# Optimization experiments

Measured on AMD Instinct MI355X. Metric: run time of the kernel, lower is better.

The kernel has to match this reference:

```python
import jax, jax.numpy as jnp
import numpy as np

B = 16      # number of point clouds
N = 4096    # points per cloud (max after densify)
D = 3       # xyz


def setup_inputs() -> dict:
    key = jax.random.key(0)
    k1, k2 = jax.random.split(key)
    pred = jax.random.normal(k1, (B * N, D), dtype=jnp.float32)
    target = jax.random.normal(k2, (B * N, D), dtype=jnp.float32)
    # sorted segment ids, equal-sized clouds (faithful to to_dense_batch usage)
    batch = jnp.repeat(jnp.arange(B, dtype=jnp.int64), N)
    return {"pred": pred, "target": target, "batch": batch}


def to_dense_batch(x, batch, num_batches, max_n):
    # PyG to_dense_batch: scatter flat points into [B, max_n, D], zero-padded.
    ones = jnp.ones_like(batch)
    counts = jax.ops.segment_sum(ones, batch, num_segments=num_batches)
    offsets = jnp.concatenate([jnp.zeros((1,), batch.dtype), jnp.cumsum(counts)[:-1]])
    pos = jnp.arange(batch.shape[0], dtype=batch.dtype) - offsets[batch]
    dense = jnp.zeros((num_batches, max_n, x.shape[-1]), x.dtype)
    return dense.at[batch, pos].set(x)


def chamfer_distance(x, y):
    # squared-euclidean pairwise distances via the GEMM identity
    x2 = jnp.sum(x * x, axis=-1)                      # [B, N]
    y2 = jnp.sum(y * y, axis=-1)                      # [B, M]
    xy = jnp.einsum('bnd,bmd->bnm', x, y)             # [B, N, M]
    d = x2[:, :, None] + y2[:, None, :] - 2.0 * xy    # [B, N, M]
    cham_x = jnp.mean(jnp.min(d, axis=2), axis=1)     # mean over N of min over M
    cham_y = jnp.mean(jnp.min(d, axis=1), axis=1)     # mean over M of min over N
    # point_reduction='mean', batch_reduction='mean' (pytorch3d defaults)
    return jnp.mean(cham_x + cham_y)


def reference(pred, target, batch):
    x = to_dense_batch(pred, batch, B, N)
    y = to_dense_batch(target, batch, B, N)
    return chamfer_distance(x, y)
```

## Files before the change

### kernel.cpp

```cpp
#include <hip/hip_runtime.h>


namespace {

constexpr int kB = 16;
constexpr int kN = 4096;
constexpr int kPlane = kB * kN;
constexpr int kStage = 512;
constexpr int kNS = kN / kStage;
constexpr float kScale = 1.0f / (float)(kB * kN);

typedef short bf16x8 __attribute__((ext_vector_type(8)));
typedef float f32x4 __attribute__((ext_vector_type(4)));
typedef unsigned short u16;

__device__ inline u16 bf16_rn(float f) {
  union { float f; unsigned u; } v; v.f = f;
  unsigned r = v.u + 0x7fffu + ((v.u >> 16) & 1u);
  return (u16)(r >> 16);
}
__device__ inline float bf16_f(u16 h) {
  union { unsigned u; float f; } v; v.u = (unsigned)h << 16;
  return v.f;
}
__device__ inline unsigned pk2(u16 lo, u16 hi) {
  return (unsigned)lo | ((unsigned)hi << 16);
}

__global__ void init_out(float* out) { out[0] = 0.0f; }

__global__ __launch_bounds__(256) void cd_prep(
    const float* __restrict__ pred, const float* __restrict__ targ,
    u16* __restrict__ Apred, u16* __restrict__ Atarg,
    u16* __restrict__ Bpred, u16* __restrict__ Btarg,
    float* __restrict__ out) {
  const int p = blockIdx.x * 256 + threadIdx.x;
  if (p == 0) out[0] = 0.0f;
  const int cloud = p >> 12, q = p & (kN - 1);
  const int stg = q >> 9, pl = q & (kStage - 1);
  const size_t boff = (size_t)cloud * 65536 + (size_t)stg * 8192 + (size_t)pl * 8;
  const u16 one = 0x3F80;

  const float* srcs[2] = {pred, targ};
  u16* adsts[2] = {Apred, Atarg};
  u16* bdsts[2] = {Bpred, Btarg};
#pragma unroll
  for (int which = 0; which < 2; ++which) {
    const float a = srcs[which][3 * p], c = srcs[which][3 * p + 1],
                d = srcs[which][3 * p + 2];
    const u16 ah = bf16_rn(a), ch = bf16_rn(c), dh = bf16_rn(d);
    const u16 al = bf16_rn(a - bf16_f(ah));
    const u16 cl = bf16_rn(c - bf16_f(ch));
    const u16 dl = bf16_rn(d - bf16_f(dh));
    const float s2 = fmaf(a, a, fmaf(c, c, d * d));
    const u16 s2h = bf16_rn(s2);
    const u16 s2l = bf16_rn(s2 - bf16_f(s2h));
    {
      uint4 w0, w1;
      w0.x = pk2(ah, ch); w0.y = pk2(dh, al); w0.z = pk2(cl, dl); w0.w = pk2(ah, ch);
      w1.x = pk2(dh, al); w1.y = pk2(cl, dl); w1.z = pk2(s2h, s2l); w1.w = pk2(one, one);
      uint4* dst = reinterpret_cast<uint4*>(adsts[which] + (size_t)p * 16);
      dst[0] = w0; dst[1] = w1;
    }
    {
      const u16 nah = bf16_rn(-2.0f * bf16_f(ah));
      const u16 nch = bf16_rn(-2.0f * bf16_f(ch));
      const u16 ndh = bf16_rn(-2.0f * bf16_f(dh));
      const u16 nal = bf16_rn(-2.0f * bf16_f(al));
      const u16 ncl = bf16_rn(-2.0f * bf16_f(cl));
      const u16 ndl = bf16_rn(-2.0f * bf16_f(dl));
      uint4 w0, w1;
      w0.x = pk2(nah, nch); w0.y = pk2(ndh, nah); w0.z = pk2(nch, ndh); w0.w = pk2(nal, ncl);
      w1.x = pk2(ndl, nal); w1.y = pk2(ncl, ndl); w1.z = pk2(one, one); w1.w = pk2(s2h, s2l);
      *reinterpret_cast<uint4*>(bdsts[which] + boff) = w0;
      *reinterpret_cast<uint4*>(bdsts[which] + boff + 4096) = w1;
    }
  }
}

__global__ __launch_bounds__(256) void cd_mfma(
    const u16* __restrict__ Apred, const u16* __restrict__ Atarg,
    const u16* __restrict__ Bpred, const u16* __restrict__ Btarg,
    float* __restrict__ out) {
  __shared__ uint4 Blds4[2052];
  __shared__ float wsum[4];

  const int t = threadIdx.x;
  const int w = t >> 6, lane = t & 63;
  const int l15 = lane & 15, kg = lane >> 4;
  const bool act = (kg < 2);
  const int g = kg & 1;
  const int chunk = blockIdx.x;
  const int cloud = blockIdx.y;
  const int dir = blockIdx.z;
  const u16* __restrict__ A = dir ? Atarg : Apred;
  const u16* __restrict__ B = dir ? Bpred : Btarg;

  const int arow0 = cloud * kN + chunk * 128 + w * 32 + l15;
  union { uint4 u; bf16x8 v; } af0, af1;
  af0.u = make_uint4(0, 0, 0, 0);
  af1.u = make_uint4(0, 0, 0, 0);
  if (act) {
    af0.u = *reinterpret_cast<const uint4*>(A + (size_t)arow0 * 16 + g * 8);
    af1.u = *reinterpret_cast<const uint4*>(A + (size_t)(arow0 + 16) * 16 + g * 8);
  }

  const char* bcloud = (const char*)B + (size_t)cloud * 131072;
  char* ldsbase = (char*)Blds4;
#define STAGE(st, buf)                                                        \
  {                                                                           \
    const char* _src = bcloud + (size_t)(st) * 16384;                         \
    char* _dst = ldsbase + (buf) * 16384;                                     \
    _Pragma("unroll")                                                         \
    for (int i = 0; i < 4; ++i) {                                             \
      __builtin_amdgcn_global_load_lds(                                       \
          (const __attribute__((address_space(1))) void*)(_src +              \
              ((w * 4 + i) * 64 + lane) * 16),                                \
          (__attribute__((address_space(3))) void*)(_dst + (w * 4 + i) * 1024),\
          16, 0, 0);                                                          \
    }                                                                         \
  }

  const int rb0 = act ? (g * 8192 + l15 * 16) : 32768;
  const int rstep = act ? 256 : 0;
  const int bufstep = act ? 16384 : 0;

  f32x4 z4;
#pragma unroll
  for (int r = 0; r < 4; ++r) z4[r] = 0.0f;
  float rmin0[4], rmin1[4];
#pragma unroll
  for (int r = 0; r < 4; ++r) { rmin0[r] = 1e30f; rmin1[r] = 1e30f; }

  STAGE(0, 0);
  if (t == 0) Blds4[2048] = make_uint4(0, 0, 0, 0);
  __syncthreads();

  for (int st = 0; st < kNS; ++st) {
    if (st < kNS - 1) STAGE(st + 1, (st + 1) & 1);
    const char* pb = ldsbase + rb0 + (st & 1) * bufstep;
#pragma unroll 4
    for (int jt = 0; jt < kStage / 16; ++jt) {
      union { uint4 u; bf16x8 v; } bu;
      bu.u = *reinterpret_cast<const uint4*>(pb);
      pb += rstep;
      const f32x4 s0 =
          __builtin_amdgcn_mfma_f32_16x16x32_bf16(af0.v, bu.v, z4, 0, 0, 0);
      const f32x4 s1 =
          __builtin_amdgcn_mfma_f32_16x16x32_bf16(af1.v, bu.v, z4, 0, 0, 0);
#pragma unroll
      for (int r = 0; r < 4; ++r) {
        rmin0[r] = fminf(rmin0[r], s0[r]);
        rmin1[r] = fminf(rmin1[r], s1[r]);
      }
    }
    __syncthreads();
  }
#undef STAGE

#pragma unroll
  for (int sh = 1; sh < 16; sh <<= 1) {
#pragma unroll
    for (int r = 0; r < 4; ++r) {
      rmin0[r] = fminf(rmin0[r], __shfl_xor(rmin0[r], sh, 64));
      rmin1[r] = fminf(rmin1[r], __shfl_xor(rmin1[r], sh, 64));
    }
  }
  float s = 0.0f;
#pragma unroll
  for (int r = 0; r < 4; ++r) s += rmin0[r] + rmin1[r];
  s = (l15 == 0) ? s : 0.0f;
  s += __shfl_xor(s, 16, 64);
  s += __shfl_xor(s, 32, 64);
  if (lane == 0) wsum[w] = s;
  __syncthreads();
  if (t == 0)
    atomicAdd(out, (wsum[0] + wsum[1] + wsum[2] + wsum[3]) * kScale);
}

template <int KX>
__global__ __launch_bounds__(256) void chamfer_direct(
    const float* __restrict__ pred, const float* __restrict__ targ,
    float* __restrict__ out) {
  __shared__ float4 tA[128], tB[128];
  const int t = threadIdx.x;
  const int xb = blockIdx.x, b = blockIdx.y, dir = blockIdx.z;
  const float* __restrict__ X = dir ? targ : pred;
  const float* __restrict__ Y = dir ? pred : targ;
  float2 xx2[KX], xy2[KX], xz2[KX];
  float x2[KX], mn[KX];
  const int ibase = b * kN + xb * (256 * KX) + t;
#pragma unroll
  for (int k = 0; k < KX; ++k) {
    const int i = ibase + k * 256;
    const float a = X[3 * i], c = X[3 * i + 1], d = X[3 * i + 2];
    x2[k] = fmaf(a, a, fmaf(c, c, d * d));
    xx2[k] = make_float2(-2.0f * a, -2.0f * a);
    xy2[k] = make_float2(-2.0f * c, -2.0f * c);
    xz2[k] = make_float2(-2.0f * d, -2.0f * d);
    mn[k] = 1e30f;
  }
  for (int t0 = 0; t0 < kN; t0 += 256) {
    __syncthreads();
    if (t < 128) {
      const int j0 = 3 * (b * kN + t0 + 2 * t);
      const float a0 = Y[j0], c0 = Y[j0 + 1], d0 = Y[j0 + 2];
      const float a1 = Y[j0 + 3], c1 = Y[j0 + 4], d1 = Y[j0 + 5];
      tA[t] = make_float4(a0, a1, c0, c1);
      tB[t] = make_float4(d0, d1, fmaf(a0, a0, fmaf(c0, c0, d0 * d0)),
                          fmaf(a1, a1, fmaf(c1, c1, d1 * d1)));
    }
    __syncthreads();
    for (int jj = 0; jj < 128; ++jj) {
      const float4 qa = tA[jj], qb = tB[jj];
      const float2 qx = make_float2(qa.x, qa.y), qy = make_float2(qa.z, qa.w);
      const float2 qz = make_float2(qb.x, qb.y), qw = make_float2(qb.z, qb.w);
#pragma unroll
      for (int k = 0; k < KX; ++k) {
        float2 acc;
        asm("v_pk_fma_f32 %0, %1, %2, %3\n\t"
            "v_pk_fma_f32 %0, %4, %5, %0\n\t"
            "v_pk_fma_f32 %0, %6, %7, %0"
            : "=&v"(acc)
            : "v"(xz2[k]), "v"(qz), "v"(qw), "v"(xy2[k]), "v"(qy),
              "v"(xx2[k]), "v"(qx));
        asm("v_min3_f32 %0, %0, %1, %2" : "+v"(mn[k]) : "v"(acc.x), "v"(acc.y));
      }
    }
  }
  float s = 0.0f;
#pragma unroll
  for (int k = 0; k < KX; ++k) s += x2[k] + mn[k];
  for (int o = 32; o > 0; o >>= 1) s += __shfl_down(s, o, 64);
  __shared__ float wsum[4];
  const int lane = t & 63, wv = t >> 6;
  if (lane == 0) wsum[wv] = s;
  __syncthreads();
  if (t == 0)
    atomicAdd(out, (wsum[0] + wsum[1] + wsum[2] + wsum[3]) * kScale);
}

}

extern "C" void kernel_launch(void* const* d_in, const int* in_sizes, int n_in,
                              void* d_out, int out_size, void* d_ws,
                              size_t ws_size, hipStream_t stream) {
  const float* pred = (const float*)d_in[0];
  const float* targ = (const float*)d_in[1];
  float* out = (float*)d_out;

  const size_t needOne = (size_t)kPlane * 16 * sizeof(u16);
  if (ws_size >= 4 * needOne) {
    u16* Apred = (u16*)d_ws;
    u16* Atarg = (u16*)((char*)d_ws + needOne);
    u16* Bpred = (u16*)((char*)d_ws + 2 * needOne);
    u16* Btarg = (u16*)((char*)d_ws + 3 * needOne);
    cd_prep<<<dim3(kPlane / 256), 256, 0, stream>>>(pred, targ, Apred, Atarg,
                                                    Bpred, Btarg, out);
    cd_mfma<<<dim3(32, kB, 2), 256, 0, stream>>>(Apred, Atarg, Bpred, Btarg,
                                                 out);
  } else {
    init_out<<<dim3(1), dim3(1), 0, stream>>>(out);
    constexpr int KX = 8;
    dim3 grid(kN / (256 * KX), kB, 2);
    chamfer_direct<KX><<<grid, 256, 0, stream>>>(pred, targ, out);
  }
}
```

Baseline: 100.5 us.

## Split MFMA chamfer inner dimension across 4 slices with separate min-reduce kernel

Splits each cloud's target points into four slices so the MFMA kernel launches four times as many blocks, each scanning a quarter of the columns with half-sized LDS stages. Per-row partial minima go to a workspace buffer, and a new reduce kernel takes the min across slices, sums the results and atomically accumulates into the output. The aim is more parallelism and occupancy on a grid of 1024 blocks, which leaves many CUs idle or poorly latency-hidden. The cost is an extra kernel launch, extra global traffic for the partials, and a larger workspace requirement that could trigger the slow fallback path.

Result: slower. 106.4 us (+5.8%).

```diff
diff --git a/kernel.cpp b/kernel.cpp
--- a/kernel.cpp
+++ b/kernel.cpp
@@ -6,8 +6,9 @@
 constexpr int kB = 16;
 constexpr int kN = 4096;
 constexpr int kPlane = kB * kN;
-constexpr int kStage = 512;
-constexpr int kNS = kN / kStage;
+constexpr int kJS = 4;
+constexpr int kStage = 256;
+constexpr int kNS = (kN / kJS) / kStage;
 constexpr float kScale = 1.0f / (float)(kB * kN);
 
 typedef short bf16x8 __attribute__((ext_vector_type(8)));
@@ -37,8 +38,8 @@
   const int p = blockIdx.x * 256 + threadIdx.x;
   if (p == 0) out[0] = 0.0f;
   const int cloud = p >> 12, q = p & (kN - 1);
-  const int stg = q >> 9, pl = q & (kStage - 1);
-  const size_t boff = (size_t)cloud * 65536 + (size_t)stg * 8192 + (size_t)pl * 8;
+  const int stg = q >> 8, pl = q & (kStage - 1);
+  const size_t boff = (size_t)cloud * 65536 + (size_t)stg * 4096 + (size_t)pl * 8;
   const u16 one = 0x3F80;
 
   const float* srcs[2] = {pred, targ};
@@ -73,7 +74,7 @@
       w0.x = pk2(nah, nch); w0.y = pk2(ndh, nah); w0.z = pk2(nch, ndh); w0.w = pk2(nal, ncl);
       w1.x = pk2(ndl, nal); w1.y = pk2(ncl, ndl); w1.z = pk2(one, one); w1.w = pk2(s2h, s2l);
       *reinterpret_cast<uint4*>(bdsts[which] + boff) = w0;
-      *reinterpret_cast<uint4*>(bdsts[which] + boff + 4096) = w1;
+      *reinterpret_cast<uint4*>(bdsts[which] + boff + 2048) = w1;
     }
   }
 }
@@ -81,16 +82,17 @@
 __global__ __launch_bounds__(256) void cd_mfma(
     const u16* __restrict__ Apred, const u16* __restrict__ Atarg,
     const u16* __restrict__ Bpred, const u16* __restrict__ Btarg,
-    float* __restrict__ out) {
-  __shared__ uint4 Blds4[2052];
-  __shared__ float wsum[4];
+    float* __restrict__ rowpart) {
+  __shared__ uint4 Blds4[1028];
 
   const int t = threadIdx.x;
   const int w = t >> 6, lane = t & 63;
   const int l15 = lane & 15, kg = lane >> 4;
   const bool act = (kg < 2);
   const int g = kg & 1;
-  const int chunk = blockIdx.x;
+  const int bx = blockIdx.x;
+  const int chunk = bx & 31;
+  const int slice = bx >> 5;
   const int cloud = blockIdx.y;
   const int dir = blockIdx.z;
   const u16* __restrict__ A = dir ? Atarg : Apred;
@@ -105,25 +107,25 @@
     af1.u = *reinterpret_cast<const uint4*>(A + (size_t)(arow0 + 16) * 16 + g * 8);
   }
 
-  const char* bcloud = (const char*)B + (size_t)cloud * 131072;
+  const char* bsl = (const char*)B + (size_t)cloud * 131072 + (size_t)slice * 32768;
   char* ldsbase = (char*)Blds4;
 #define STAGE(st, buf)                                                        \
   {                                                                           \
-    const char* _src = bcloud + (size_t)(st) * 16384;                         \
-    char* _dst = ldsbase + (buf) * 16384;                                     \
+    const char* _src = bsl + (size_t)(st) * 8192;                             \
+    char* _dst = ldsbase + (buf) * 8192;                                      \
     _Pragma("unroll")                                                         \
-    for (int i = 0; i < 4; ++i) {                                             \
+    for (int i = 0; i < 2; ++i) {                                             \
       __builtin_amdgcn_global_load_lds(                                       \
           (const __attribute__((address_space(1))) void*)(_src +              \
-              ((w * 4 + i) * 64 + lane) * 16),                                \
-          (__attribute__((address_space(3))) void*)(_dst + (w * 4 + i) * 1024),\
+              ((w * 2 + i) * 64 + lane) * 16),                                \
+          (__attribute__((address_space(3))) void*)(_dst + (w * 2 + i) * 1024),\
           16, 0, 0);                                                          \
     }                                                                         \
   }
 
-  const int rb0 = act ? (g * 8192 + l15 * 16) : 32768;
+  const int rb0 = act ? (g * 4096 + l15 * 16) : 16384;
   const int rstep = act ? 256 : 0;
-  const int bufstep = act ? 16384 : 0;
+  const int bufstep = act ? 8192 : 0;
 
   f32x4 z4;
 #pragma unroll
@@ -133,7 +135,7 @@
   for (int r = 0; r < 4; ++r) { rmin0[r] = 1e30f; rmin1[r] = 1e30f; }
 
   STAGE(0, 0);
-  if (t == 0) Blds4[2048] = make_uint4(0, 0, 0, 0);
+  if (t == 0) Blds4[1024] = make_uint4(0, 0, 0, 0);
   __syncthreads();
 
   for (int st = 0; st < kNS; ++st) {
@@ -166,15 +168,33 @@
       rmin1[r] = fminf(rmin1[r], __shfl_xor(rmin1[r], sh, 64));
     }
   }
-  float s = 0.0f;
-#pragma unroll
-  for (int r = 0; r < 4; ++r) s += rmin0[r] + rmin1[r];
-  s = (l15 == 0) ? s : 0.0f;
-  s += __shfl_xor(s, 16, 64);
-  s += __shfl_xor(s, 32, 64);
-  if (lane == 0) wsum[w] = s;
+  if (l15 == 0) {
+    float* rp = rowpart + (((size_t)dir * kJS + slice) * kB + cloud) * kN +
+                chunk * 128 + w * 32;
+#pragma unroll
+    for (int r = 0; r < 4; ++r) {
+      rp[kg * 4 + r] = rmin0[r];
+      rp[16 + kg * 4 + r] = rmin1[r];
+    }
+  }
+}
+
+__global__ __launch_bounds__(256) void cd_reduce(
+    const float* __restrict__ rowpart, float* __restrict__ out) {
+  const int u = blockIdx.x * 256 + threadIdx.x;
+  const int dir = u >> 16, rest = u & 65535;
+  const int cloud = rest >> 12, row = rest & (kN - 1);
+  float rm = 1e30f;
+#pragma unroll
+  for (int s2 = 0; s2 < kJS; ++s2)
+    rm = fminf(rm, rowpart[(((size_t)dir * kJS + s2) * kB + cloud) * kN + row]);
+  float s = rm;
+  for (int o = 32; o > 0; o >>= 1) s += __shfl_down(s, o, 64);
+  __shared__ float wsum[4];
+  const int lane = threadIdx.x & 63, wv = threadIdx.x >> 6;
+  if (lane == 0) wsum[wv] = s;
   __syncthreads();
-  if (t == 0)
+  if (threadIdx.x == 0)
     atomicAdd(out, (wsum[0] + wsum[1] + wsum[2] + wsum[3]) * kScale);
 }
 
@@ -250,15 +270,20 @@
   float* out = (float*)d_out;
 
   const size_t needOne = (size_t)kPlane * 16 * sizeof(u16);
-  if (ws_size >= 4 * needOne) {
+  const size_t needRow = (size_t)2 * kJS * kPlane * sizeof(float) / kB * kB;
+  const size_t needRowB = (size_t)2 * kJS * kB * kN * sizeof(float);
+  (void)needRow;
+  if (ws_size >= 4 * needOne + needRowB) {
     u16* Apred = (u16*)d_ws;
     u16* Atarg = (u16*)((char*)d_ws + needOne);
     u16* Bpred = (u16*)((char*)d_ws + 2 * needOne);
     u16* Btarg = (u16*)((char*)d_ws + 3 * needOne);
+    float* rowpart = (float*)((char*)d_ws + 4 * needOne);
     cd_prep<<<dim3(kPlane / 256), 256, 0, stream>>>(pred, targ, Apred, Atarg,
                                                     Bpred, Btarg, out);
-    cd_mfma<<<dim3(32, kB, 2), 256, 0, stream>>>(Apred, Atarg, Bpred, Btarg,
-                                                 out);
+    cd_mfma<<<dim3(32 * kJS, kB, 2), 256, 0, stream>>>(Apred, Atarg, Bpred,
+                                                       Btarg, rowpart);
+    cd_reduce<<<dim3(2 * kPlane / 256), 256, 0, stream>>>(rowpart, out);
   } else {
     init_out<<<dim3(1), dim3(1), 0, stream>>>(out);
     constexpr int KX = 8;
```

## Stream B fragments directly from global memory instead of LDS double-buffering

Applied to the files above, without the earlier changes.

Drops the LDS staging of the B operand via global_load_lds with double buffering and block-wide barriers. Each wave instead loads its own B fragments straight from global/L2 into registers with a two-deep software prefetch, and issues four MFMAs per pair of loads. The prep kernel now writes B in plain row-major order to match. This removes LDS traffic and __syncthreads, at the cost of each wave re-reading B from cache, which raises global/L2 load pressure and register use.

New measurement: 124.0 us. 1.23x slower.

```diff
diff --git a/kernel.cpp b/kernel.cpp
--- a/kernel.cpp
+++ b/kernel.cpp
@@ -6,8 +6,6 @@
 constexpr int kB = 16;
 constexpr int kN = 4096;
 constexpr int kPlane = kB * kN;
-constexpr int kStage = 512;
-constexpr int kNS = kN / kStage;
 constexpr float kScale = 1.0f / (float)(kB * kN);
 
 typedef short bf16x8 __attribute__((ext_vector_type(8)));
@@ -36,9 +34,6 @@
     float* __restrict__ out) {
   const int p = blockIdx.x * 256 + threadIdx.x;
   if (p == 0) out[0] = 0.0f;
-  const int cloud = p >> 12, q = p & (kN - 1);
-  const int stg = q >> 9, pl = q & (kStage - 1);
-  const size_t boff = (size_t)cloud * 65536 + (size_t)stg * 8192 + (size_t)pl * 8;
   const u16 one = 0x3F80;
 
   const float* srcs[2] = {pred, targ};
@@ -72,8 +67,8 @@
       uint4 w0, w1;
       w0.x = pk2(nah, nch); w0.y = pk2(ndh, nah); w0.z = pk2(nch, ndh); w0.w = pk2(nal, ncl);
       w1.x = pk2(ndl, nal); w1.y = pk2(ncl, ndl); w1.z = pk2(one, one); w1.w = pk2(s2h, s2l);
-      *reinterpret_cast<uint4*>(bdsts[which] + boff) = w0;
-      *reinterpret_cast<uint4*>(bdsts[which] + boff + 4096) = w1;
+      uint4* dst = reinterpret_cast<uint4*>(bdsts[which] + (size_t)p * 16);
+      dst[0] = w0; dst[1] = w1;
     }
   }
 }
@@ -82,7 +77,6 @@
     const u16* __restrict__ Apred, const u16* __restrict__ Atarg,
     const u16* __restrict__ Bpred, const u16* __restrict__ Btarg,
     float* __restrict__ out) {
-  __shared__ uint4 Blds4[2052];
   __shared__ float wsum[4];
 
   const int t = threadIdx.x;
@@ -97,7 +91,8 @@
   const u16* __restrict__ B = dir ? Bpred : Btarg;
 
   const int arow0 = cloud * kN + chunk * 128 + w * 32 + l15;
-  union { uint4 u; bf16x8 v; } af0, af1;
+  union U { uint4 u; bf16x8 v; };
+  U af0, af1;
   af0.u = make_uint4(0, 0, 0, 0);
   af1.u = make_uint4(0, 0, 0, 0);
   if (act) {
@@ -105,25 +100,14 @@
     af1.u = *reinterpret_cast<const uint4*>(A + (size_t)(arow0 + 16) * 16 + g * 8);
   }
 
-  const char* bcloud = (const char*)B + (size_t)cloud * 131072;
-  char* ldsbase = (char*)Blds4;
-#define STAGE(st, buf)                                                        \
-  {                                                                           \
-    const char* _src = bcloud + (size_t)(st) * 16384;                         \
-    char* _dst = ldsbase + (buf) * 16384;                                     \
-    _Pragma("unroll")                                                         \
-    for (int i = 0; i < 4; ++i) {                                             \
-      __builtin_amdgcn_global_load_lds(                                       \
-          (const __attribute__((address_space(1))) void*)(_src +              \
-              ((w * 4 + i) * 64 + lane) * 16),                                \
-          (__attribute__((address_space(3))) void*)(_dst + (w * 4 + i) * 1024),\
-          16, 0, 0);                                                          \
-    }                                                                         \
-  }
-
-  const int rb0 = act ? (g * 8192 + l15 * 16) : 32768;
-  const int rstep = act ? 256 : 0;
-  const int bufstep = act ? 16384 : 0;
+  const char* bb = (const char*)(B + (size_t)cloud * kN * 16);
+  const int lofs = l15 * 32 + g * 16;
+
+#define LDF(JB, U0, U1)                                                      \
+  if (act) {                                                                 \
+    U0.u = *reinterpret_cast<const uint4*>(bb + (size_t)(JB) * 32 + lofs);   \
+    U1.u = *reinterpret_cast<const uint4*>(bb + (size_t)(JB) * 32 + 512 + lofs); \
+  }
 
   f32x4 z4;
 #pragma unroll
@@ -132,31 +116,41 @@
 #pragma unroll
   for (int r = 0; r < 4; ++r) { rmin0[r] = 1e30f; rmin1[r] = 1e30f; }
 
-  STAGE(0, 0);
-  if (t == 0) Blds4[2048] = make_uint4(0, 0, 0, 0);
-  __syncthreads();
-
-  for (int st = 0; st < kNS; ++st) {
-    if (st < kNS - 1) STAGE(st + 1, (st + 1) & 1);
-    const char* pb = ldsbase + rb0 + (st & 1) * bufstep;
-#pragma unroll 4
-    for (int jt = 0; jt < kStage / 16; ++jt) {
-      union { uint4 u; bf16x8 v; } bu;
-      bu.u = *reinterpret_cast<const uint4*>(pb);
-      pb += rstep;
-      const f32x4 s0 =
-          __builtin_amdgcn_mfma_f32_16x16x32_bf16(af0.v, bu.v, z4, 0, 0, 0);
-      const f32x4 s1 =
-          __builtin_amdgcn_mfma_f32_16x16x32_bf16(af1.v, bu.v, z4, 0, 0, 0);
-#pragma unroll
-      for (int r = 0; r < 4; ++r) {
-        rmin0[r] = fminf(rmin0[r], s0[r]);
-        rmin1[r] = fminf(rmin1[r], s1[r]);
-      }
-    }
-    __syncthreads();
-  }
-#undef STAGE
+#define CMP(U0, U1)                                                          \
+  {                                                                          \
+    const f32x4 s00 =                                                        \
+        __builtin_amdgcn_mfma_f32_16x16x32_bf16(af0.v, U0.v, z4, 0, 0, 0);   \
+    const f32x4 s01 =                                                        \
+        __builtin_amdgcn_mfma_f32_16x16x32_bf16(af0.v, U1.v, z4, 0, 0, 0);   \
+    const f32x4 s10 =                                                        \
+        __builtin_amdgcn_mfma_f32_16x16x32_bf16(af1.v, U0.v, z4, 0, 0, 0);   \
+    const f32x4 s11 =                                                        \
+        __builtin_amdgcn_mfma_f32_16x16x32_bf16(af1.v, U1.v, z4, 0, 0, 0);   \
+    _Pragma("unroll")                                                        \
+    for (int r = 0; r < 4; ++r) {                                            \
+      rmin0[r] = fminf(rmin0[r], fminf(s00[r], s01[r]));                     \
+      rmin1[r] = fminf(rmin1[r], fminf(s10[r], s11[r]));                     \
+    }                                                                        \
+  }
+
+  U c0a, c0b, c1a, c1b, n0a, n0b, n1a, n1b;
+  c0a.u = make_uint4(0, 0, 0, 0); c0b.u = c0a.u;
+  c1a.u = c0a.u; c1b.u = c0a.u;
+  n0a.u = c0a.u; n0b.u = c0a.u; n1a.u = c0a.u; n1b.u = c0a.u;
+
+  LDF(0, c0a, c0b);
+  LDF(32, c1a, c1b);
+  for (int jt = 0; jt < 128; jt += 2) {
+    const int j2 = ((jt + 2) & 127) * 32;
+    const int j3 = ((jt + 3) & 127) * 32;
+    LDF(j2, n0a, n0b);
+    CMP(c0a, c0b);
+    LDF(j3, n1a, n1b);
+    CMP(c1a, c1b);
+    c0a = n0a; c0b = n0b; c1a = n1a; c1b = n1b;
+  }
+#undef LDF
+#undef CMP
 
 #pragma unroll
   for (int sh = 1; sh < 16; sh <<= 1) {
```

## Halve per-block A tile and stage size, batch four B fragments per iteration

Applied to the files above, without the earlier changes.

Each wave now holds one 16-row A fragment instead of two, the grid doubles to 64 chunks per cloud, and the B staging buffer shrinks to 256 points. The inner loop loads four B fragments at once and issues four independent MFMAs, combining them with a min tree. The aim is more blocks for better CU occupancy and more independent MFMA work per iteration. The cost is that each B tile is reused half as much, so B traffic from global memory into LDS doubles, and there are twice as many stage barriers.

Result: slower. 108.2 us (+7.7%).

```diff
diff --git a/kernel.cpp b/kernel.cpp
--- a/kernel.cpp
+++ b/kernel.cpp
@@ -6,7 +6,7 @@
 constexpr int kB = 16;
 constexpr int kN = 4096;
 constexpr int kPlane = kB * kN;
-constexpr int kStage = 512;
+constexpr int kStage = 256;
 constexpr int kNS = kN / kStage;
 constexpr float kScale = 1.0f / (float)(kB * kN);
 
@@ -37,8 +37,8 @@
   const int p = blockIdx.x * 256 + threadIdx.x;
   if (p == 0) out[0] = 0.0f;
   const int cloud = p >> 12, q = p & (kN - 1);
-  const int stg = q >> 9, pl = q & (kStage - 1);
-  const size_t boff = (size_t)cloud * 65536 + (size_t)stg * 8192 + (size_t)pl * 8;
+  const int stg = q >> 8, pl = q & (kStage - 1);
+  const size_t boff = (size_t)cloud * 65536 + (size_t)stg * 4096 + (size_t)pl * 8;
   const u16 one = 0x3F80;
 
   const float* srcs[2] = {pred, targ};
@@ -73,7 +73,7 @@
       w0.x = pk2(nah, nch); w0.y = pk2(ndh, nah); w0.z = pk2(nch, ndh); w0.w = pk2(nal, ncl);
       w1.x = pk2(ndl, nal); w1.y = pk2(ncl, ndl); w1.z = pk2(one, one); w1.w = pk2(s2h, s2l);
       *reinterpret_cast<uint4*>(bdsts[which] + boff) = w0;
-      *reinterpret_cast<uint4*>(bdsts[which] + boff + 4096) = w1;
+      *reinterpret_cast<uint4*>(bdsts[which] + boff + 2048) = w1;
     }
   }
 }
@@ -82,7 +82,7 @@
     const u16* __restrict__ Apred, const u16* __restrict__ Atarg,
     const u16* __restrict__ Bpred, const u16* __restrict__ Btarg,
     float* __restrict__ out) {
-  __shared__ uint4 Blds4[2052];
+  __shared__ uint4 Blds4[1028];
   __shared__ float wsum[4];
 
   const int t = threadIdx.x;
@@ -96,62 +96,68 @@
   const u16* __restrict__ A = dir ? Atarg : Apred;
   const u16* __restrict__ B = dir ? Bpred : Btarg;
 
-  const int arow0 = cloud * kN + chunk * 128 + w * 32 + l15;
-  union { uint4 u; bf16x8 v; } af0, af1;
+  const int arow0 = cloud * kN + chunk * 64 + w * 16 + l15;
+  union U { uint4 u; bf16x8 v; };
+  U af0;
   af0.u = make_uint4(0, 0, 0, 0);
-  af1.u = make_uint4(0, 0, 0, 0);
-  if (act) {
+  if (act)
     af0.u = *reinterpret_cast<const uint4*>(A + (size_t)arow0 * 16 + g * 8);
-    af1.u = *reinterpret_cast<const uint4*>(A + (size_t)(arow0 + 16) * 16 + g * 8);
-  }
-
-  const char* bcloud = (const char*)B + (size_t)cloud * 131072;
+
+  const char* bcl = (const char*)B + (size_t)cloud * 131072;
   char* ldsbase = (char*)Blds4;
 #define STAGE(st, buf)                                                        \
   {                                                                           \
-    const char* _src = bcloud + (size_t)(st) * 16384;                         \
-    char* _dst = ldsbase + (buf) * 16384;                                     \
+    const char* _src = bcl + (size_t)(st) * 8192;                             \
+    char* _dst = ldsbase + (buf) * 8192;                                      \
     _Pragma("unroll")                                                         \
-    for (int i = 0; i < 4; ++i) {                                             \
+    for (int i = 0; i < 2; ++i) {                                             \
       __builtin_amdgcn_global_load_lds(                                       \
           (const __attribute__((address_space(1))) void*)(_src +              \
-              ((w * 4 + i) * 64 + lane) * 16),                                \
-          (__attribute__((address_space(3))) void*)(_dst + (w * 4 + i) * 1024),\
+              ((w * 2 + i) * 64 + lane) * 16),                                \
+          (__attribute__((address_space(3))) void*)(_dst + (w * 2 + i) * 1024),\
           16, 0, 0);                                                          \
     }                                                                         \
   }
 
-  const int rb0 = act ? (g * 8192 + l15 * 16) : 32768;
+  const int rb0 = act ? (g * 4096 + l15 * 16) : 16384;
   const int rstep = act ? 256 : 0;
-  const int bufstep = act ? 16384 : 0;
+  const int bufstep = act ? 8192 : 0;
 
   f32x4 z4;
 #pragma unroll
   for (int r = 0; r < 4; ++r) z4[r] = 0.0f;
-  float rmin0[4], rmin1[4];
-#pragma unroll
-  for (int r = 0; r < 4; ++r) { rmin0[r] = 1e30f; rmin1[r] = 1e30f; }
+  float rmin[4];
+#pragma unroll
+  for (int r = 0; r < 4; ++r) rmin[r] = 1e30f;
 
   STAGE(0, 0);
-  if (t == 0) Blds4[2048] = make_uint4(0, 0, 0, 0);
+  if (t == 0) Blds4[1024] = make_uint4(0, 0, 0, 0);
   __syncthreads();
 
   for (int st = 0; st < kNS; ++st) {
     if (st < kNS - 1) STAGE(st + 1, (st + 1) & 1);
     const char* pb = ldsbase + rb0 + (st & 1) * bufstep;
-#pragma unroll 4
-    for (int jt = 0; jt < kStage / 16; ++jt) {
-      union { uint4 u; bf16x8 v; } bu;
-      bu.u = *reinterpret_cast<const uint4*>(pb);
-      pb += rstep;
+#pragma unroll
+    for (int bt = 0; bt < kStage / 64; ++bt) {
+      U b0, b1, b2, b3;
+      b0.u = *reinterpret_cast<const uint4*>(pb);
+      b1.u = *reinterpret_cast<const uint4*>(pb + rstep);
+      b2.u = *reinterpret_cast<const uint4*>(pb + 2 * rstep);
+      b3.u = *reinterpret_cast<const uint4*>(pb + 3 * rstep);
+      pb += 4 * rstep;
       const f32x4 s0 =
-          __builtin_amdgcn_mfma_f32_16x16x32_bf16(af0.v, bu.v, z4, 0, 0, 0);
+          __builtin_amdgcn_mfma_f32_16x16x32_bf16(af0.v, b0.v, z4, 0, 0, 0);
       const f32x4 s1 =
-          __builtin_amdgcn_mfma_f32_16x16x32_bf16(af1.v, bu.v, z4, 0, 0, 0);
+          __builtin_amdgcn_mfma_f32_16x16x32_bf16(af0.v, b1.v, z4, 0, 0, 0);
+      const f32x4 s2 =
+          __builtin_amdgcn_mfma_f32_16x16x32_bf16(af0.v, b2.v, z4, 0, 0, 0);
+      const f32x4 s3 =
+          __builtin_amdgcn_mfma_f32_16x16x32_bf16(af0.v, b3.v, z4, 0, 0, 0);
 #pragma unroll
       for (int r = 0; r < 4; ++r) {
-        rmin0[r] = fminf(rmin0[r], s0[r]);
-        rmin1[r] = fminf(rmin1[r], s1[r]);
+        const float m01 = fminf(s0[r], s1[r]);
+        const float m23 = fminf(s2[r], s3[r]);
+        rmin[r] = fminf(rmin[r], fminf(m01, m23));
       }
     }
     __syncthreads();
@@ -161,14 +167,12 @@
 #pragma unroll
   for (int sh = 1; sh < 16; sh <<= 1) {
 #pragma unroll
-    for (int r = 0; r < 4; ++r) {
-      rmin0[r] = fminf(rmin0[r], __shfl_xor(rmin0[r], sh, 64));
-      rmin1[r] = fminf(rmin1[r], __shfl_xor(rmin1[r], sh, 64));
-    }
+    for (int r = 0; r < 4; ++r)
+      rmin[r] = fminf(rmin[r], __shfl_xor(rmin[r], sh, 64));
   }
   float s = 0.0f;
 #pragma unroll
-  for (int r = 0; r < 4; ++r) s += rmin0[r] + rmin1[r];
+  for (int r = 0; r < 4; ++r) s += rmin[r];
   s = (l15 == 0) ? s : 0.0f;
   s += __shfl_xor(s, 16, 64);
   s += __shfl_xor(s, 32, 64);
@@ -257,7 +261,7 @@
     u16* Btarg = (u16*)((char*)d_ws + 3 * needOne);
     cd_prep<<<dim3(kPlane / 256), 256, 0, stream>>>(pred, targ, Apred, Atarg,
                                                     Bpred, Btarg, out);
-    cd_mfma<<<dim3(32, kB, 2), 256, 0, stream>>>(Apred, Atarg, Bpred, Btarg,
+    cd_mfma<<<dim3(64, kB, 2), 256, 0, stream>>>(Apred, Atarg, Bpred, Btarg,
                                                  out);
   } else {
     init_out<<<dim3(1), dim3(1), 0, stream>>>(out);
```
